# Kernel optimization log

Measured on AMD Instinct MI355X. Metric: run time of the kernel, lower is better.

## Reference

```python
import jax, jax.numpy as jnp
import numpy as np

NUM_GRAPHS = 2048
NODES_PER_GRAPH = 256
N_NODES = NUM_GRAPHS * NODES_PER_GRAPH
N_EDGES = 2 * N_NODES
F_IN = 768
HID = 128
N_CLS = 2


def setup_inputs() -> dict:
    key = jax.random.key(0)
    ks = jax.random.split(key, 12)
    x = jax.random.normal(ks[0], (N_NODES, F_IN), dtype=jnp.float32)
    edge_index = jax.random.randint(ks[1], (2, N_EDGES), 0, N_NODES, dtype=jnp.int32)
    batch = jnp.repeat(jnp.arange(NUM_GRAPHS, dtype=jnp.int32), NODES_PER_GRAPH)
    s = 1.0 / np.sqrt(F_IN)
    sh = 1.0 / np.sqrt(HID)
    s2h = 1.0 / np.sqrt(2 * HID)
    return {
        "x": x,
        "edge_index": edge_index,
        "batch": batch,
        # SAGEConv: lin_l (aggregated neighbors, with bias) + lin_r (root, no bias)
        "W_l": jax.random.uniform(ks[2], (F_IN, HID), jnp.float32, -s, s),
        "b_l": jax.random.uniform(ks[3], (HID,), jnp.float32, -s, s),
        "W_r": jax.random.uniform(ks[4], (F_IN, HID), jnp.float32, -s, s),
        "W0": jax.random.uniform(ks[5], (F_IN, HID), jnp.float32, -s, s),
        "b0": jax.random.uniform(ks[6], (HID,), jnp.float32, -s, s),
        "W1": jax.random.uniform(ks[7], (2 * HID, HID), jnp.float32, -s2h, s2h),
        "b1": jax.random.uniform(ks[8], (HID,), jnp.float32, -s2h, s2h),
        "W2": jax.random.uniform(ks[9], (HID, N_CLS), jnp.float32, -sh, sh),
        "b2": jax.random.uniform(ks[10], (HID,), jnp.float32, -sh, sh)[:N_CLS],
    }


def reference(x, edge_index, batch, W_l, b_l, W_r, W0, b0, W1, b1, W2, b2):
    n = x.shape[0]
    src, dst = edge_index[0], edge_index[1]
    # SAGEConv with mean aggregation: gather -> segment mean -> transform
    msg_sum = jax.ops.segment_sum(x[src], dst, num_segments=n)      # [N, F]
    cnt = jax.ops.segment_sum(jnp.ones((src.shape[0],), x.dtype), dst, num_segments=n)
    agg = msg_sum / jnp.maximum(cnt, 1.0)[:, None]
    h = jax.nn.relu(agg @ W_l + b_l + x @ W_r)                       # [N, H]
    # global max pool per graph
    pooled = jax.ops.segment_max(h, batch, num_segments=NUM_GRAPHS)  # [G, H]
    # root (news) node = first node of each graph (batch is sorted)
    roots = jnp.searchsorted(batch, jnp.arange(NUM_GRAPHS, dtype=batch.dtype))
    news = jax.nn.relu(x[roots] @ W0 + b0)                           # [G, H]
    z = jax.nn.relu(jnp.concatenate([pooled, news], axis=1) @ W1 + b1)
    return jax.nn.log_softmax(z @ W2 + b2, axis=-1)                  # [G, 2]
```

## Files before the change

### kernel.cpp

```cpp
#include <hip/hip_runtime.h>

#define NGRAPH 2048
#define NPG 256
#define NNODE (NGRAPH*NPG)
#define NEDGE (2*NNODE)
#define FIN 768
#define HID 128
#define SLOTS 64
#define BK 32
#define NKT (FIN/BK)

typedef __bf16 bf16x8 __attribute__((ext_vector_type(8)));
typedef __bf16 bf16x4 __attribute__((ext_vector_type(4)));
typedef float f32x4 __attribute__((ext_vector_type(4)));

__device__ __forceinline__ float bflo(unsigned v) {
    return __uint_as_float((v & 0xffffu) << 16);
}
__device__ __forceinline__ float bfhi(unsigned v) {
    return __uint_as_float(v & 0xffff0000u);
}

__global__ __launch_bounds__(256) void k_prep(
    const float* __restrict__ Wl, const float* __restrict__ Wr,
    const float* __restrict__ W0, __bf16* __restrict__ WbT,
    int* __restrict__ deg)
{
    int idx = blockIdx.x * 256 + threadIdx.x;
    deg[idx] = 0;
    if (idx < 384 * FIN) {
        int n = idx / FIN;
        int k = idx - n * FIN;
        float v;
        if (n < HID)            v = Wl[k * HID + n];
        else if (n < 2 * HID)   v = Wr[k * HID + (n - HID)];
        else                    v = W0[k * HID + (n - 2 * HID)];
        WbT[idx] = (__bf16)v;
    }
}

__global__ __launch_bounds__(512, 1) void k_gemm(
    const float* __restrict__ X, const __bf16* __restrict__ WbT,
    __bf16* __restrict__ Yl, __bf16* __restrict__ Yr,
    const int* __restrict__ ei, int* __restrict__ deg, int* __restrict__ elist)
{
    __shared__ __align__(16) char sm[65536];
    const int t = threadIdx.x;

    {
        int e = blockIdx.x * 512 + t;
        int src = ei[e];
        int dst = ei[NEDGE + e];
        int pos = atomicAdd(deg + dst, 1);
        if (pos < SLOTS) elist[(size_t)pos * NNODE + dst] = src;
    }

    const int lane = t & 63;
    const int w = t >> 6;
    const int wr = w >> 2;
    const int wc = w & 3;
    const size_t node0 = (size_t)blockIdx.x * 256;

    f32x4 acc[8][4];
#pragma unroll
    for (int m = 0; m < 8; ++m)
#pragma unroll
        for (int n = 0; n < 4; ++n)
            acc[m][n] = (f32x4){0.f, 0.f, 0.f, 0.f};

    const int arow = t >> 1;
    const int ak = (t & 1) * 16;
    const float* asrc = X + (node0 + arow) * FIN + ak;
    const int axr = ((arow >> 1) & 3) << 4;
    const int aoff0 = arow * 64 + ((ak * 2) ^ axr);
    const int aoff1 = arow * 64 + ((ak * 2 + 16) ^ axr);

#define STAGE_B(k0, dst)                                                    \
    {                                                                       \
        _Pragma("unroll")                                                   \
        for (int r = 0; r < 2; ++r) {                                       \
            int idx = r * 512 + t;                                          \
            int bn = idx >> 2;                                              \
            int bj = idx & 3;                                               \
            int koff = (bj ^ ((bn >> 1) & 3)) << 3;                         \
            const __bf16* g = WbT + bn * FIN + (k0) + koff;                 \
            __builtin_amdgcn_global_load_lds(                               \
                (__attribute__((address_space(1))) void*)g,                 \
                (__attribute__((address_space(3))) void*)((dst) + idx * 16),\
                16, 0, 0);                                                  \
        }                                                                   \
    }

    {
        const f32x4* s4 = (const f32x4*)asrc;
        f32x4 p0 = s4[0], p1 = s4[1], p2 = s4[2], p3 = s4[3];
        STAGE_B(0, sm + 32768);
        bf16x8 h0, h1;
#pragma unroll
        for (int i = 0; i < 4; ++i) {
            h0[i]     = (__bf16)p0[i];
            h0[4 + i] = (__bf16)p1[i];
            h1[i]     = (__bf16)p2[i];
            h1[4 + i] = (__bf16)p3[i];
        }
        *(bf16x8*)(sm + aoff0) = h0;
        *(bf16x8*)(sm + aoff1) = h1;
    }
    __syncthreads();

    int cur = 0;
    for (int kt = 0; kt < NKT; ++kt) {
        char* sAc = sm + cur * 16384;
        char* sBc = sm + 32768 + cur * 16384;
        char* sAn = sm + (cur ^ 1) * 16384;
        char* sBn = sm + 32768 + (cur ^ 1) * 16384;
        const bool more = (kt + 1 < NKT);

        f32x4 q0, q1, q2, q3;
        if (more) {
            const f32x4* s4 = (const f32x4*)(asrc + (kt + 1) * BK);
            q0 = s4[0]; q1 = s4[1]; q2 = s4[2]; q3 = s4[3];
            STAGE_B((kt + 1) * BK, sBn);
        }

        const int kb = (lane >> 4) << 4;
        bf16x8 a[8], b[4];
#pragma unroll
        for (int m = 0; m < 8; ++m) {
            int row = wr * 128 + m * 16 + (lane & 15);
            a[m] = *(const bf16x8*)(sAc + row * 64 + (kb ^ (((row >> 1) & 3) << 4)));
        }
#pragma unroll
        for (int n = 0; n < 4; ++n) {
            int row = wc * 64 + n * 16 + (lane & 15);
            b[n] = *(const bf16x8*)(sBc + row * 64 + (kb ^ (((row >> 1) & 3) << 4)));
        }
#pragma unroll
        for (int m = 0; m < 8; ++m)
#pragma unroll
            for (int n = 0; n < 4; ++n)
                acc[m][n] = __builtin_amdgcn_mfma_f32_16x16x32_bf16(
                    a[m], b[n], acc[m][n], 0, 0, 0);

        if (more) {
            bf16x8 h0, h1;
#pragma unroll
            for (int i = 0; i < 4; ++i) {
                h0[i]     = (__bf16)q0[i];
                h0[4 + i] = (__bf16)q1[i];
                h1[i]     = (__bf16)q2[i];
                h1[4 + i] = (__bf16)q3[i];
            }
            *(bf16x8*)(sAn + aoff0) = h0;
            *(bf16x8*)(sAn + aoff1) = h1;
        }
        __syncthreads();
        cur ^= 1;
    }

#pragma unroll
    for (int m = 0; m < 8; ++m) {
        const int rbase = wr * 128 + m * 16 + ((lane >> 4) << 2);
#pragma unroll
        for (int n = 0; n < 4; ++n) {
            const int col = wc * 64 + n * 16 + (lane & 15);
            __bf16* dst = (col < HID) ? Yl : Yr;
            const int c = col & (HID - 1);
#pragma unroll
            for (int j = 0; j < 4; ++j)
                dst[(node0 + rbase + j) * HID + c] = (__bf16)acc[m][n][j];
        }
    }
#undef STAGE_B
}

__global__ __launch_bounds__(512) void k_news(
    const float* __restrict__ X, const __bf16* __restrict__ W0bT,
    const float* __restrict__ b0, float* __restrict__ news)
{
    __shared__ __align__(16) char sm[12288];
    const int t = threadIdx.x;
    const int lane = t & 63;
    const int w = t >> 6;
    const int wr = w >> 2;
    const int wc = w & 3;
    const int g0 = blockIdx.x * 64;

    f32x4 acc[2][2];
#pragma unroll
    for (int m = 0; m < 2; ++m)
#pragma unroll
        for (int n = 0; n < 2; ++n)
            acc[m][n] = (f32x4){0.f, 0.f, 0.f, 0.f};

    const int arow = t >> 3;
    const int ak = (t & 7) * 4;
    const float* asrc = X + (size_t)(g0 + arow) * (NPG * FIN) + ak;
    const int aoff = arow * 64 + (((ak * 2) ^ (((arow >> 1) & 3) << 4)));

    for (int kt = 0; kt < NKT; ++kt) {
        const int k0 = kt * BK;
        __syncthreads();
        {
            f32x4 p = *(const f32x4*)(asrc + k0);
            bf16x4 h;
#pragma unroll
            for (int i = 0; i < 4; ++i) h[i] = (__bf16)p[i];
            *(bf16x4*)(sm + aoff) = h;
        }
        {
            int bn = t >> 2;
            int bj = t & 3;
            int koff = (bj ^ ((bn >> 1) & 3)) << 3;
            const __bf16* g = W0bT + bn * FIN + k0 + koff;
            __builtin_amdgcn_global_load_lds(
                (__attribute__((address_space(1))) void*)g,
                (__attribute__((address_space(3))) void*)(sm + 4096 + t * 16),
                16, 0, 0);
        }
        __syncthreads();

        const int kb = (lane >> 4) << 4;
        bf16x8 a[2], b[2];
#pragma unroll
        for (int m = 0; m < 2; ++m) {
            int row = wr * 32 + m * 16 + (lane & 15);
            a[m] = *(const bf16x8*)(sm + row * 64 + (kb ^ (((row >> 1) & 3) << 4)));
        }
#pragma unroll
        for (int n = 0; n < 2; ++n) {
            int row = wc * 32 + n * 16 + (lane & 15);
            b[n] = *(const bf16x8*)(sm + 4096 + row * 64 + (kb ^ (((row >> 1) & 3) << 4)));
        }
#pragma unroll
        for (int m = 0; m < 2; ++m)
#pragma unroll
            for (int n = 0; n < 2; ++n)
                acc[m][n] = __builtin_amdgcn_mfma_f32_16x16x32_bf16(
                    a[m], b[n], acc[m][n], 0, 0, 0);
    }

#pragma unroll
    for (int m = 0; m < 2; ++m) {
        const int rbase = wr * 32 + m * 16 + ((lane >> 4) << 2);
#pragma unroll
        for (int n = 0; n < 2; ++n) {
            const int col = wc * 32 + n * 16 + (lane & 15);
            const float bb = b0[col];
#pragma unroll
            for (int j = 0; j < 4; ++j)
                news[(size_t)(g0 + rbase + j) * HID + col] =
                    fmaxf(acc[m][n][j] + bb, 0.f);
        }
    }
}

__global__ __launch_bounds__(512) void k_fused(
    const int* __restrict__ deg, const int* __restrict__ elist,
    const __bf16* __restrict__ Yl, const __bf16* __restrict__ Yr,
    const float* __restrict__ bl, const float* __restrict__ news,
    const float* __restrict__ W1, const float* __restrict__ b1,
    const float* __restrict__ W2, const float* __restrict__ b2,
    float* __restrict__ out)
{
    __shared__ int   sdeg[NPG];
    __shared__ int   sel[4 * NPG];
    __shared__ float red[8 * HID];
    __shared__ float cat[2 * HID];
    __shared__ float zs[HID];

    const int g = blockIdx.x;
    const int t = threadIdx.x;
    const size_t gbase = (size_t)g * NPG;

    if (t < NPG) sdeg[t] = deg[gbase + t];
#pragma unroll
    for (int r = 0; r < 2; ++r) {
        int idx = r * 512 + t;
        sel[idx] = elist[(size_t)(idx >> 8) * NNODE + gbase + (idx & 255)];
    }
    __syncthreads();

    const int l = t & 63;
    const int sub = t >> 6;
    const int half = l >> 5;
    const int lj = l & 31;
    const int d4 = lj * 4;
    const float4 blv = *(const float4*)(bl + d4);
    const uint2* yl2 = (const uint2*)Yl;
    const uint2* yr2 = (const uint2*)Yr;

    float m0 = -3.0e38f, m1 = -3.0e38f, m2 = -3.0e38f, m3 = -3.0e38f;

    for (int k4 = 0; k4 < 8; ++k4) {
        const int nA = sub + 8 * (4 * k4 + half);
        const int nB = sub + 8 * (4 * k4 + 2 + half);
        const int dgA = sdeg[nA], dgB = sdeg[nB];
        int sA[4], sB[4];
#pragma unroll
        for (int j = 0; j < 4; ++j) {
            int cA = sel[j * NPG + nA];
            int cB = sel[j * NPG + nB];
            sA[j] = (j < dgA) ? cA : 0;
            sB[j] = (j < dgB) ? cB : 0;
        }
        uint2 vA[4], vB[4];
#pragma unroll
        for (int j = 0; j < 4; ++j) {
            vA[j] = yl2[(size_t)sA[j] * 32 + lj];
            vB[j] = yl2[(size_t)sB[j] * 32 + lj];
        }
        const uint2 yA = yr2[(gbase + nA) * 32 + lj];
        const uint2 yB = yr2[(gbase + nB) * 32 + lj];

        float s0A = 0.f, s1A = 0.f, s2A = 0.f, s3A = 0.f;
        float s0B = 0.f, s1B = 0.f, s2B = 0.f, s3B = 0.f;
#pragma unroll
        for (int j = 0; j < 4; ++j) {
            const float mA = (j < dgA) ? 1.f : 0.f;
            const float mB = (j < dgB) ? 1.f : 0.f;
            s0A = fmaf(mA, bflo(vA[j].x), s0A);
            s1A = fmaf(mA, bfhi(vA[j].x), s1A);
            s2A = fmaf(mA, bflo(vA[j].y), s2A);
            s3A = fmaf(mA, bfhi(vA[j].y), s3A);
            s0B = fmaf(mB, bflo(vB[j].x), s0B);
            s1B = fmaf(mB, bfhi(vB[j].x), s1B);
            s2B = fmaf(mB, bflo(vB[j].y), s2B);
            s3B = fmaf(mB, bfhi(vB[j].y), s3B);
        }
        int mx = dgA > dgB ? dgA : dgB;
        mx = max(mx, __shfl_xor(mx, 32));
        mx = mx < SLOTS ? mx : SLOTS;
        for (int j = 4; j < mx; ++j) {
            int cA = elist[(size_t)j * NNODE + gbase + nA];
            int cB = elist[(size_t)j * NNODE + gbase + nB];
            int eA = (j < dgA) ? cA : 0;
            int eB = (j < dgB) ? cB : 0;
            uint2 wA = yl2[(size_t)eA * 32 + lj];
            uint2 wB = yl2[(size_t)eB * 32 + lj];
            const float mA = (j < dgA) ? 1.f : 0.f;
            const float mB = (j < dgB) ? 1.f : 0.f;
            s0A = fmaf(mA, bflo(wA.x), s0A);
            s1A = fmaf(mA, bfhi(wA.x), s1A);
            s2A = fmaf(mA, bflo(wA.y), s2A);
            s3A = fmaf(mA, bfhi(wA.y), s3A);
            s0B = fmaf(mB, bflo(wB.x), s0B);
            s1B = fmaf(mB, bfhi(wB.x), s1B);
            s2B = fmaf(mB, bflo(wB.y), s2B);
            s3B = fmaf(mB, bfhi(wB.y), s3B);
        }
        const float invA = 1.f / fmaxf((float)dgA, 1.f);
        const float invB = 1.f / fmaxf((float)dgB, 1.f);
        float h0 = fmaf(s0A, invA, blv.x) + bflo(yA.x);
        float h1 = fmaf(s1A, invA, blv.y) + bfhi(yA.x);
        float h2 = fmaf(s2A, invA, blv.z) + bflo(yA.y);
        float h3 = fmaf(s3A, invA, blv.w) + bfhi(yA.y);
        m0 = fmaxf(m0, fmaxf(h0, 0.f));
        m1 = fmaxf(m1, fmaxf(h1, 0.f));
        m2 = fmaxf(m2, fmaxf(h2, 0.f));
        m3 = fmaxf(m3, fmaxf(h3, 0.f));
        h0 = fmaf(s0B, invB, blv.x) + bflo(yB.x);
        h1 = fmaf(s1B, invB, blv.y) + bfhi(yB.x);
        h2 = fmaf(s2B, invB, blv.z) + bflo(yB.y);
        h3 = fmaf(s3B, invB, blv.w) + bfhi(yB.y);
        m0 = fmaxf(m0, fmaxf(h0, 0.f));
        m1 = fmaxf(m1, fmaxf(h1, 0.f));
        m2 = fmaxf(m2, fmaxf(h2, 0.f));
        m3 = fmaxf(m3, fmaxf(h3, 0.f));
    }
    m0 = fmaxf(m0, __shfl_xor(m0, 32));
    m1 = fmaxf(m1, __shfl_xor(m1, 32));
    m2 = fmaxf(m2, __shfl_xor(m2, 32));
    m3 = fmaxf(m3, __shfl_xor(m3, 32));
    if (half == 0) {
        float4 mv = {m0, m1, m2, m3};
        *(float4*)(red + sub * HID + d4) = mv;
    }
    __syncthreads();

    if (t < HID) {
        float v = red[t];
#pragma unroll
        for (int s = 1; s < 8; ++s) v = fmaxf(v, red[s * HID + t]);
        cat[t] = v;
        cat[HID + t] = news[(size_t)g * HID + t];
    }
    __syncthreads();

    if (t < HID) {
        float a0 = 0.f, a1 = 0.f, a2 = 0.f, a3 = 0.f;
        for (int k = 0; k < 2 * HID; k += 4) {
            a0 = fmaf(cat[k + 0], W1[(k + 0) * HID + t], a0);
            a1 = fmaf(cat[k + 1], W1[(k + 1) * HID + t], a1);
            a2 = fmaf(cat[k + 2], W1[(k + 2) * HID + t], a2);
            a3 = fmaf(cat[k + 3], W1[(k + 3) * HID + t], a3);
        }
        zs[t] = fmaxf((a0 + a1) + (a2 + a3) + b1[t], 0.f);
    }
    __syncthreads();

    if (t < 64) {
        float z0 = zs[t * 2], z1 = zs[t * 2 + 1];
        float p0 = fmaf(z0, W2[t * 4 + 0], z1 * W2[t * 4 + 2]);
        float p1 = fmaf(z0, W2[t * 4 + 1], z1 * W2[t * 4 + 3]);
#pragma unroll
        for (int off = 32; off; off >>= 1) {
            p0 += __shfl_down(p0, off);
            p1 += __shfl_down(p1, off);
        }
        if (t == 0) {
            float l0 = p0 + b2[0], l1 = p1 + b2[1];
            float mx = fmaxf(l0, l1);
            float lse = mx + logf(expf(l0 - mx) + expf(l1 - mx));
            out[(size_t)g * 2 + 0] = l0 - lse;
            out[(size_t)g * 2 + 1] = l1 - lse;
        }
    }
}

extern "C" void kernel_launch(void* const* d_in, const int* in_sizes, int n_in,
                              void* d_out, int out_size, void* d_ws, size_t ws_size,
                              hipStream_t stream)
{
    const float* x   = (const float*)d_in[0];
    const int*   ei  = (const int*)d_in[1];
    const float* W_l = (const float*)d_in[3];
    const float* b_l = (const float*)d_in[4];
    const float* W_r = (const float*)d_in[5];
    const float* W0  = (const float*)d_in[6];
    const float* b0  = (const float*)d_in[7];
    const float* W1  = (const float*)d_in[8];
    const float* b1  = (const float*)d_in[9];
    const float* W2  = (const float*)d_in[10];
    const float* b2  = (const float*)d_in[11];
    float* out = (float*)d_out;

    char* ws = (char*)d_ws;
    size_t off = 0;
    auto alloc = [&](size_t bytes) {
        char* p = ws + off;
        off += (bytes + 511) & ~(size_t)511;
        return p;
    };
    __bf16* WbT   = (__bf16*)alloc((size_t)384 * FIN * 2);
    __bf16* Yl    = (__bf16*)alloc((size_t)NNODE * HID * 2);
    __bf16* Yr    = (__bf16*)alloc((size_t)NNODE * HID * 2);
    int*    deg   = (int*)alloc((size_t)NNODE * 4);
    int*    elist = (int*)alloc((size_t)NNODE * SLOTS * 4);
    float*  news  = (float*)alloc((size_t)NGRAPH * HID * 4);
    if (off > ws_size) return;

    k_prep<<<NNODE / 256, 256, 0, stream>>>(W_l, W_r, W0, WbT, deg);
    k_gemm<<<NNODE / 256, 512, 0, stream>>>(x, WbT, Yl, Yr, ei, deg, elist);
    k_news<<<NGRAPH / 64, 512, 0, stream>>>(x, WbT + (size_t)256 * FIN, b0, news);
    k_fused<<<NGRAPH, 512, 0, stream>>>(deg, elist, Yl, Yr, b_l, news,
                                        W1, b1, W2, b2, out);
}
```

Before: 649.2 us.

## Deepen GEMM pipeline with register prefetch two tiles ahead and manual waitcnts

Restructures the k_gemm main loop so the fp32 A-tile loads for k-tile t+2 are issued while computing tile t, with the bf16 conversion and LDS write of tile t+1 happening before the MFMAs. B tiles are staged via global_load_lds one tile ahead. __syncthreads is replaced by explicit s_waitcnt vmcnt/lgkmcnt plus s_barrier, so only the older loads are waited on and the newer ones stay in flight. This aims to hide global load latency better, at the cost of more live registers and fragile hand-tuned waitcnt counts.

```diff
diff --git a/kernel.cpp b/kernel.cpp
--- a/kernel.cpp
+++ b/kernel.cpp
@@ -39,6 +39,70 @@
     }
 }
 
+template<int VMC, bool HASB, bool HASA, bool HASW>
+__device__ __forceinline__ void gemm_tile(
+    const char* rbuf, char* wbuf, int t, int lane, int wr, int wc,
+    const float* asrc, const __bf16* WbT, int ktB, int ktA,
+    f32x4& c0, f32x4& c1, f32x4& c2, f32x4& c3,
+    f32x4& i0, f32x4& i1, f32x4& i2, f32x4& i3,
+    int aoff0, int aoff1, f32x4 (&acc)[8][4])
+{
+    if constexpr (HASB) {
+#pragma unroll
+        for (int r = 0; r < 2; ++r) {
+            int idx = r * 512 + t;
+            int bn = idx >> 2, bj = idx & 3;
+            int koff = (bj ^ ((bn >> 1) & 3)) << 3;
+            const __bf16* g = WbT + bn * FIN + ktB * BK + koff;
+            __builtin_amdgcn_global_load_lds(
+                (__attribute__((address_space(1))) void*)g,
+                (__attribute__((address_space(3))) void*)(wbuf + 16384 + idx * 16),
+                16, 0, 0);
+        }
+        __builtin_amdgcn_sched_barrier(0);
+    }
+    if constexpr (HASA) {
+        const f32x4* s4 = (const f32x4*)(asrc + ktA * BK);
+        i0 = s4[0]; i1 = s4[1]; i2 = s4[2]; i3 = s4[3];
+    }
+    if constexpr (HASW) {
+        bf16x8 h0, h1;
+#pragma unroll
+        for (int i = 0; i < 4; ++i) {
+            h0[i]     = (__bf16)c0[i];
+            h0[4 + i] = (__bf16)c1[i];
+            h1[i]     = (__bf16)c2[i];
+            h1[4 + i] = (__bf16)c3[i];
+        }
+        *(bf16x8*)(wbuf + aoff0) = h0;
+        *(bf16x8*)(wbuf + aoff1) = h1;
+    }
+    const int kb = (lane >> 4) << 4;
+    bf16x8 a[8], b[4];
+#pragma unroll
+    for (int m = 0; m < 8; ++m) {
+        int row = wr * 128 + m * 16 + (lane & 15);
+        a[m] = *(const bf16x8*)(rbuf + row * 64 + (kb ^ (((row >> 1) & 3) << 4)));
+    }
+#pragma unroll
+    for (int n = 0; n < 4; ++n) {
+        int row = wc * 64 + n * 16 + (lane & 15);
+        b[n] = *(const bf16x8*)(rbuf + 16384 + row * 64 + (kb ^ (((row >> 1) & 3) << 4)));
+    }
+#pragma unroll
+    for (int m = 0; m < 8; ++m)
+#pragma unroll
+        for (int n = 0; n < 4; ++n)
+            acc[m][n] = __builtin_amdgcn_mfma_f32_16x16x32_bf16(
+                a[m], b[n], acc[m][n], 0, 0, 0);
+    if constexpr (VMC == 4) asm volatile("s_waitcnt vmcnt(4)" ::: "memory");
+    else if constexpr (VMC == 0) asm volatile("s_waitcnt vmcnt(0)" ::: "memory");
+    if constexpr (VMC >= 0) {
+        asm volatile("s_waitcnt lgkmcnt(0)" ::: "memory");
+        __builtin_amdgcn_s_barrier();
+    }
+}
+
 __global__ __launch_bounds__(512, 1) void k_gemm(
     const float* __restrict__ X, const __bf16* __restrict__ WbT,
     __bf16* __restrict__ Yl, __bf16* __restrict__ Yr,
@@ -54,6 +118,7 @@
         int pos = atomicAdd(deg + dst, 1);
         if (pos < SLOTS) elist[(size_t)pos * NNODE + dst] = src;
     }
+    asm volatile("s_waitcnt vmcnt(0)" ::: "memory");
 
     const int lane = t & 63;
     const int w = t >> 6;
@@ -75,88 +140,59 @@
     const int aoff0 = arow * 64 + ((ak * 2) ^ axr);
     const int aoff1 = arow * 64 + ((ak * 2 + 16) ^ axr);
 
-#define STAGE_B(k0, dst)                                                    \
-    {                                                                       \
-        _Pragma("unroll")                                                   \
-        for (int r = 0; r < 2; ++r) {                                       \
-            int idx = r * 512 + t;                                          \
-            int bn = idx >> 2;                                              \
-            int bj = idx & 3;                                               \
-            int koff = (bj ^ ((bn >> 1) & 3)) << 3;                         \
-            const __bf16* g = WbT + bn * FIN + (k0) + koff;                 \
-            __builtin_amdgcn_global_load_lds(                               \
-                (__attribute__((address_space(1))) void*)g,                 \
-                (__attribute__((address_space(3))) void*)((dst) + idx * 16),\
-                16, 0, 0);                                                  \
-        }                                                                   \
-    }
+    char* buf0 = sm;
+    char* buf1 = sm + 32768;
+    f32x4 qa0, qa1, qa2, qa3;
+    f32x4 qb0, qb1, qb2, qb3;
 
     {
-        const f32x4* s4 = (const f32x4*)asrc;
-        f32x4 p0 = s4[0], p1 = s4[1], p2 = s4[2], p3 = s4[3];
-        STAGE_B(0, sm + 32768);
+#pragma unroll
+        for (int r = 0; r < 2; ++r) {
+            int idx = r * 512 + t;
+            int bn = idx >> 2, bj = idx & 3;
+            int koff = (bj ^ ((bn >> 1) & 3)) << 3;
+            const __bf16* g = WbT + bn * FIN + 0 * BK + koff;
+            __builtin_amdgcn_global_load_lds(
+                (__attribute__((address_space(1))) void*)g,
+                (__attribute__((address_space(3))) void*)(buf0 + 16384 + idx * 16),
+                16, 0, 0);
+        }
+        __builtin_amdgcn_sched_barrier(0);
+        {
+            const f32x4* s4 = (const f32x4*)(asrc);
+            qa0 = s4[0]; qa1 = s4[1]; qa2 = s4[2]; qa3 = s4[3];
+        }
+        {
+            const f32x4* s4 = (const f32x4*)(asrc + 1 * BK);
+            qb0 = s4[0]; qb1 = s4[1]; qb2 = s4[2]; qb3 = s4[3];
+        }
         bf16x8 h0, h1;
 #pragma unroll
         for (int i = 0; i < 4; ++i) {
-            h0[i]     = (__bf16)p0[i];
-            h0[4 + i] = (__bf16)p1[i];
-            h1[i]     = (__bf16)p2[i];
-            h1[4 + i] = (__bf16)p3[i];
-        }
-        *(bf16x8*)(sm + aoff0) = h0;
-        *(bf16x8*)(sm + aoff1) = h1;
-    }
-    __syncthreads();
-
-    int cur = 0;
-    for (int kt = 0; kt < NKT; ++kt) {
-        char* sAc = sm + cur * 16384;
-        char* sBc = sm + 32768 + cur * 16384;
-        char* sAn = sm + (cur ^ 1) * 16384;
-        char* sBn = sm + 32768 + (cur ^ 1) * 16384;
-        const bool more = (kt + 1 < NKT);
-
-        f32x4 q0, q1, q2, q3;
-        if (more) {
-            const f32x4* s4 = (const f32x4*)(asrc + (kt + 1) * BK);
-            q0 = s4[0]; q1 = s4[1]; q2 = s4[2]; q3 = s4[3];
-            STAGE_B((kt + 1) * BK, sBn);
-        }
-
-        const int kb = (lane >> 4) << 4;
-        bf16x8 a[8], b[4];
-#pragma unroll
-        for (int m = 0; m < 8; ++m) {
-            int row = wr * 128 + m * 16 + (lane & 15);
-            a[m] = *(const bf16x8*)(sAc + row * 64 + (kb ^ (((row >> 1) & 3) << 4)));
-        }
-#pragma unroll
-        for (int n = 0; n < 4; ++n) {
-            int row = wc * 64 + n * 16 + (lane & 15);
-            b[n] = *(const bf16x8*)(sBc + row * 64 + (kb ^ (((row >> 1) & 3) << 4)));
-        }
-#pragma unroll
-        for (int m = 0; m < 8; ++m)
-#pragma unroll
-            for (int n = 0; n < 4; ++n)
-                acc[m][n] = __builtin_amdgcn_mfma_f32_16x16x32_bf16(
-                    a[m], b[n], acc[m][n], 0, 0, 0);
-
-        if (more) {
-            bf16x8 h0, h1;
-#pragma unroll
-            for (int i = 0; i < 4; ++i) {
-                h0[i]     = (__bf16)q0[i];
-                h0[4 + i] = (__bf16)q1[i];
-                h1[i]     = (__bf16)q2[i];
-                h1[4 + i] = (__bf16)q3[i];
-            }
-            *(bf16x8*)(sAn + aoff0) = h0;
-            *(bf16x8*)(sAn + aoff1) = h1;
-        }
-        __syncthreads();
-        cur ^= 1;
-    }
+            h0[i]     = (__bf16)qa0[i];
+            h0[4 + i] = (__bf16)qa1[i];
+            h1[i]     = (__bf16)qa2[i];
+            h1[4 + i] = (__bf16)qa3[i];
+        }
+        *(bf16x8*)(buf0 + aoff0) = h0;
+        *(bf16x8*)(buf0 + aoff1) = h1;
+        asm volatile("s_waitcnt vmcnt(4)" ::: "memory");
+        asm volatile("s_waitcnt lgkmcnt(0)" ::: "memory");
+        __builtin_amdgcn_s_barrier();
+    }
+
+    for (int kt = 0; kt < 22; kt += 2) {
+        gemm_tile<4, true, true, true>(buf0, buf1, t, lane, wr, wc, asrc, WbT,
+            kt + 1, kt + 2, qb0, qb1, qb2, qb3, qa0, qa1, qa2, qa3,
+            aoff0, aoff1, acc);
+        gemm_tile<4, true, true, true>(buf1, buf0, t, lane, wr, wc, asrc, WbT,
+            kt + 2, kt + 3, qa0, qa1, qa2, qa3, qb0, qb1, qb2, qb3,
+            aoff0, aoff1, acc);
+    }
+    gemm_tile<0, true, false, true>(buf0, buf1, t, lane, wr, wc, asrc, WbT,
+        23, 0, qb0, qb1, qb2, qb3, qa0, qa1, qa2, qa3, aoff0, aoff1, acc);
+    gemm_tile<-1, false, false, false>(buf1, buf0, t, lane, wr, wc, asrc, WbT,
+        0, 0, qa0, qa1, qa2, qa3, qb0, qb1, qb2, qb3, aoff0, aoff1, acc);
 
 #pragma unroll
     for (int m = 0; m < 8; ++m) {
@@ -171,7 +207,6 @@
                 dst[(node0 + rbase + j) * HID + c] = (__bf16)acc[m][n][j];
         }
     }
-#undef STAGE_B
 }
 
 __global__ __launch_bounds__(512) void k_news(
```

New measurement: 605.5 us. -6.7%, faster.

## Halve GEMM tile rows to raise occupancy and merge A/B LDS buffers

Applied to the files above, without the earlier changes.

Each GEMM block now handles 128 nodes instead of 256, with 4 waves' accumulators halved and LDS per block shrunk to 48KB in unified A+B double buffers. Launch bounds request 4 blocks per CU, edge bucketing uses half the threads, and a sched_barrier pins the prefetch issue order. The intent is more resident waves to hide global latency on the fp32 X stream. The cost is reloading the weight tile twice as often, and the tight register cap may cause spills.

```diff
diff --git a/kernel.cpp b/kernel.cpp
--- a/kernel.cpp
+++ b/kernel.cpp
@@ -39,16 +39,16 @@
     }
 }
 
-__global__ __launch_bounds__(512, 1) void k_gemm(
+__global__ __launch_bounds__(512, 4) void k_gemm(
     const float* __restrict__ X, const __bf16* __restrict__ WbT,
     __bf16* __restrict__ Yl, __bf16* __restrict__ Yr,
     const int* __restrict__ ei, int* __restrict__ deg, int* __restrict__ elist)
 {
-    __shared__ __align__(16) char sm[65536];
+    __shared__ __align__(16) char sm[49152];
     const int t = threadIdx.x;
 
-    {
-        int e = blockIdx.x * 512 + t;
+    if (t < 256) {
+        int e = blockIdx.x * 256 + t;
         int src = ei[e];
         int dst = ei[NEDGE + e];
         int pos = atomicAdd(deg + dst, 1);
@@ -59,108 +59,93 @@
     const int w = t >> 6;
     const int wr = w >> 2;
     const int wc = w & 3;
-    const size_t node0 = (size_t)blockIdx.x * 256;
-
-    f32x4 acc[8][4];
-#pragma unroll
-    for (int m = 0; m < 8; ++m)
+    const size_t node0 = (size_t)blockIdx.x * 128;
+
+    f32x4 acc[4][4];
+#pragma unroll
+    for (int m = 0; m < 4; ++m)
 #pragma unroll
         for (int n = 0; n < 4; ++n)
             acc[m][n] = (f32x4){0.f, 0.f, 0.f, 0.f};
 
-    const int arow = t >> 1;
-    const int ak = (t & 1) * 16;
+    const int arow = t >> 2;
+    const int ak = (t & 3) * 8;
     const float* asrc = X + (node0 + arow) * FIN + ak;
-    const int axr = ((arow >> 1) & 3) << 4;
-    const int aoff0 = arow * 64 + ((ak * 2) ^ axr);
-    const int aoff1 = arow * 64 + ((ak * 2 + 16) ^ axr);
-
-#define STAGE_B(k0, dst)                                                    \
-    {                                                                       \
-        _Pragma("unroll")                                                   \
-        for (int r = 0; r < 2; ++r) {                                       \
-            int idx = r * 512 + t;                                          \
-            int bn = idx >> 2;                                              \
-            int bj = idx & 3;                                               \
-            int koff = (bj ^ ((bn >> 1) & 3)) << 3;                         \
-            const __bf16* g = WbT + bn * FIN + (k0) + koff;                 \
-            __builtin_amdgcn_global_load_lds(                               \
-                (__attribute__((address_space(1))) void*)g,                 \
-                (__attribute__((address_space(3))) void*)((dst) + idx * 16),\
-                16, 0, 0);                                                  \
-        }                                                                   \
-    }
-
+    const int aswz = ((arow >> 1) & 3) << 4;
+    const int aoff = arow * 64 + ((ak * 2) ^ aswz);
+
+#define STAGE_B(kt, buf)                                                     \
+    {                                                                        \
+        _Pragma("unroll")                                                    \
+        for (int r = 0; r < 2; ++r) {                                        \
+            int idx = r * 512 + t;                                           \
+            int bn = idx >> 2, bj = idx & 3;                                 \
+            int koff = (bj ^ ((bn >> 1) & 3)) << 3;                          \
+            const __bf16* gp = WbT + bn * FIN + (kt) * BK + koff;            \
+            __builtin_amdgcn_global_load_lds(                                \
+                (__attribute__((address_space(1))) void*)gp,                 \
+                (__attribute__((address_space(3))) void*)((buf) + 8192 + idx * 16),\
+                16, 0, 0);                                                   \
+        }                                                                    \
+    }
+
+    f32x4 q0, q1;
+    STAGE_B(0, sm);
     {
         const f32x4* s4 = (const f32x4*)asrc;
-        f32x4 p0 = s4[0], p1 = s4[1], p2 = s4[2], p3 = s4[3];
-        STAGE_B(0, sm + 32768);
-        bf16x8 h0, h1;
-#pragma unroll
-        for (int i = 0; i < 4; ++i) {
-            h0[i]     = (__bf16)p0[i];
-            h0[4 + i] = (__bf16)p1[i];
-            h1[i]     = (__bf16)p2[i];
-            h1[4 + i] = (__bf16)p3[i];
-        }
-        *(bf16x8*)(sm + aoff0) = h0;
-        *(bf16x8*)(sm + aoff1) = h1;
+        q0 = s4[0]; q1 = s4[1];
+        bf16x8 h;
+#pragma unroll
+        for (int i = 0; i < 4; ++i) { h[i] = (__bf16)q0[i]; h[4 + i] = (__bf16)q1[i]; }
+        *(bf16x8*)(sm + aoff) = h;
     }
     __syncthreads();
 
     int cur = 0;
     for (int kt = 0; kt < NKT; ++kt) {
-        char* sAc = sm + cur * 16384;
-        char* sBc = sm + 32768 + cur * 16384;
-        char* sAn = sm + (cur ^ 1) * 16384;
-        char* sBn = sm + 32768 + (cur ^ 1) * 16384;
+        char* bufC = sm + cur * 24576;
+        char* bufN = sm + (cur ^ 1) * 24576;
         const bool more = (kt + 1 < NKT);
 
-        f32x4 q0, q1, q2, q3;
         if (more) {
+            STAGE_B(kt + 1, bufN);
             const f32x4* s4 = (const f32x4*)(asrc + (kt + 1) * BK);
-            q0 = s4[0]; q1 = s4[1]; q2 = s4[2]; q3 = s4[3];
-            STAGE_B((kt + 1) * BK, sBn);
+            q0 = s4[0]; q1 = s4[1];
+            __builtin_amdgcn_sched_barrier(0);
         }
 
         const int kb = (lane >> 4) << 4;
-        bf16x8 a[8], b[4];
-#pragma unroll
-        for (int m = 0; m < 8; ++m) {
-            int row = wr * 128 + m * 16 + (lane & 15);
-            a[m] = *(const bf16x8*)(sAc + row * 64 + (kb ^ (((row >> 1) & 3) << 4)));
+        bf16x8 a[4], b[4];
+#pragma unroll
+        for (int m = 0; m < 4; ++m) {
+            int row = wr * 64 + m * 16 + (lane & 15);
+            a[m] = *(const bf16x8*)(bufC + row * 64 + (kb ^ (((row >> 1) & 3) << 4)));
         }
 #pragma unroll
         for (int n = 0; n < 4; ++n) {
-            int row = wc * 64 + n * 16 + (lane & 15);
-            b[n] = *(const bf16x8*)(sBc + row * 64 + (kb ^ (((row >> 1) & 3) << 4)));
-        }
-#pragma unroll
-        for (int m = 0; m < 8; ++m)
+            int col = wc * 64 + n * 16 + (lane & 15);
+            b[n] = *(const bf16x8*)(bufC + 8192 + col * 64 + (kb ^ (((col >> 1) & 3) << 4)));
+        }
+#pragma unroll
+        for (int m = 0; m < 4; ++m)
 #pragma unroll
             for (int n = 0; n < 4; ++n)
                 acc[m][n] = __builtin_amdgcn_mfma_f32_16x16x32_bf16(
                     a[m], b[n], acc[m][n], 0, 0, 0);
 
         if (more) {
-            bf16x8 h0, h1;
-#pragma unroll
-            for (int i = 0; i < 4; ++i) {
-                h0[i]     = (__bf16)q0[i];
-                h0[4 + i] = (__bf16)q1[i];
-                h1[i]     = (__bf16)q2[i];
-                h1[4 + i] = (__bf16)q3[i];
-            }
-            *(bf16x8*)(sAn + aoff0) = h0;
-            *(bf16x8*)(sAn + aoff1) = h1;
+            bf16x8 h;
+#pragma unroll
+            for (int i = 0; i < 4; ++i) { h[i] = (__bf16)q0[i]; h[4 + i] = (__bf16)q1[i]; }
+            *(bf16x8*)(bufN + aoff) = h;
         }
         __syncthreads();
         cur ^= 1;
     }
 
 #pragma unroll
-    for (int m = 0; m < 8; ++m) {
-        const int rbase = wr * 128 + m * 16 + ((lane >> 4) << 2);
+    for (int m = 0; m < 4; ++m) {
+        const int rbase = wr * 64 + m * 16 + ((lane >> 4) << 2);
 #pragma unroll
         for (int n = 0; n < 4; ++n) {
             const int col = wc * 64 + n * 16 + (lane & 15);
@@ -451,7 +436,7 @@
     if (off > ws_size) return;
 
     k_prep<<<NNODE / 256, 256, 0, stream>>>(W_l, W_r, W0, WbT, deg);
-    k_gemm<<<NNODE / 256, 512, 0, stream>>>(x, WbT, Yl, Yr, ei, deg, elist);
+    k_gemm<<<NNODE / 128, 512, 0, stream>>>(x, WbT, Yl, Yr, ei, deg, elist);
     k_news<<<NGRAPH / 64, 512, 0, stream>>>(x, WbT + (size_t)256 * FIN, b0, news);
     k_fused<<<NGRAPH, 512, 0, stream>>>(deg, elist, Yl, Yr, b_l, news,
                                         W1, b1, W2, b2, out);
```

Measured after the change: 685.7 us. +5.6%, slower.
